# Kernel tuning notes

Hardware: AMD Instinct MI355X
Metric: run time of the kernel (lower is better)

## Reference

```python
import jax, jax.numpy as jnp
import numpy as np

B, D0, D1 = 4096, 128, 128
T, DEPTH, W = 64, 2, 4          # num_tree, depth, width
S = W ** (DEPTH + 1)            # num_state = 64
NODES = sum(W ** l for l in range(DEPTH + 1))  # 21 internal nodes per tree
D = D0 + D1


def setup_inputs() -> dict:
    key = jax.random.key(0)
    ks = jax.random.split(key, 9)
    inp0 = jax.random.normal(ks[0], (B, D0), jnp.float32)
    inp1 = jax.random.normal(ks[1], (B, D1), jnp.float32)
    x2 = jax.random.normal(ks[2], (B,), jnp.float32)
    # ForestLinear: per-tree, per-node linear maps to `width` branch logits
    W_nodes = 0.02 * jax.random.normal(ks[3], (T, NODES, D, W), jnp.float32)
    b_nodes = jnp.zeros((T, NODES, W), jnp.float32)
    # MultiDense([0,1], 1): per-(tree,state) linear probe per input
    W0 = 0.02 * jax.random.normal(ks[4], (T, S, D0), jnp.float32)
    b0 = jnp.zeros((T, S), jnp.float32)
    W1 = 0.02 * jax.random.normal(ks[5], (T, S, D1), jnp.float32)
    b1 = jnp.zeros((T, S), jnp.float32)
    return {"inp0": inp0, "inp1": inp1, "x2": x2,
            "W_nodes": W_nodes, "b_nodes": b_nodes,
            "W0": W0, "b0": b0, "W1": W1, "b1": b1}


def _forest_states(x, W_nodes, b_nodes):
    # x: [B, D] -> leaf-state probabilities [B, T, S]
    logits = jnp.einsum('bd,tndw->btnw', x, W_nodes) + b_nodes  # [B,T,NODES,W]
    probs = jax.nn.softmax(logits, axis=-1)
    p = jnp.ones((x.shape[0], T, 1), probs.dtype)
    off = 0
    for l in range(DEPTH + 1):
        n = W ** l
        pl = probs[:, :, off:off + n, :]                 # [B,T,n,W]
        p = (p[..., None] * pl).reshape(x.shape[0], T, n * W)
        off += n
    return p  # [B, T, S]


def reference(inp0, inp1, x2, W_nodes, b_nodes, W0, b0, W1, b1):
    x_states = _forest_states(jnp.concatenate([inp0, inp1], axis=-1), W_nodes, b_nodes)
    # per-tree/state linear probes; equivalent to tile + MultiDense, no materialized tile
    x_pred = (jnp.einsum('bd,tsd->bts', inp0, W0) + b0
              + jnp.einsum('bd,tsd->bts', inp1, W1) + b1)  # [B,T,S]
    y_pred_logit_parallel = x2[:, None, None] + x_pred
    ave_pred_tree = jnp.sum(x_states * jax.nn.sigmoid(y_pred_logit_parallel), axis=2)  # [B,T]
    ave_pred = jnp.mean(ave_pred_tree, axis=1)  # [B]
    return (y_pred_logit_parallel, ave_pred)
```

## Files before the change

### kernel.cpp

```cpp
#include <hip/hip_runtime.h>

#define B_SZ    4096
#define DD      256
#define T_TREES 64
#define NNODES  21
#define S_LEAF  64
#define M_TILE  128
#define HBYTES  40960
#define WBYTES  (2 * HBYTES)
#define XOFF    ((size_t)T_TREES * WBYTES)
#define QBYTES  20480


typedef __attribute__((ext_vector_type(8))) short  short8;
typedef __attribute__((ext_vector_type(4))) float  f32x4;

#define DPP_ADD(x, ctrl) ((x) + __int_as_float(__builtin_amdgcn_mov_dpp(__float_as_int(x), (ctrl), 0xF, 0xF, true)))
#define DPP_MOV(x, ctrl) __int_as_float(__builtin_amdgcn_mov_dpp(__float_as_int(x), (ctrl), 0xF, 0xF, true))
__device__ __forceinline__ float qsum4(float x) {
    x = DPP_ADD(x, 0xB1);
    x = DPP_ADD(x, 0x4E);
    return x;
}
__device__ __forceinline__ float rsum16(float x) {
    x = DPP_ADD(x, 0xB1);
    x = DPP_ADD(x, 0x4E);
    x = DPP_ADD(x, 0x124);
    x = DPP_ADD(x, 0x128);
    return x;
}

__device__ __forceinline__ unsigned short f2bf(float f) {
    unsigned int u = __float_as_uint(f);
    u += 0x7fffu + ((u >> 16) & 1u);
    return (unsigned short)(u >> 16);
}
__device__ __forceinline__ void gl2lds16(const void* g, void* l) {
    __builtin_amdgcn_global_load_lds(
        (const __attribute__((address_space(1))) unsigned int*)g,
        (__attribute__((address_space(3))) unsigned int*)l, 16, 0, 0);
}
__device__ __host__ __forceinline__ int woffh(int c, int klo) {
    return c * 256 + (((klo ^ c) & 15) << 4);
}
__device__ __host__ __forceinline__ int woffq(int c, int klo) {
    return (c >> 1) * 256 + (((((klo << 1) ^ (c & 14))) | (c & 1)) << 4);
}

__global__ void zero_ave_kernel(float* __restrict__ out1) {
    int i = blockIdx.x * 256 + threadIdx.x;
    if (i < B_SZ) out1[i] = 0.0f;
}

__global__ void prep_weights(const float* __restrict__ Wn, const float* __restrict__ W0,
                             const float* __restrict__ W1, const float* __restrict__ inp0,
                             const float* __restrict__ inp1, char* __restrict__ ws,
                             float* __restrict__ out1) {
    int id = blockIdx.x * 256 + threadIdx.x;
    if (id < 43008) {
        int oct  = id & 31;
        int rest = id >> 5;
        int n    = rest % NNODES;
        int t    = rest / NNODES;
        int h    = oct >> 4, klo = oct & 15;
        const f32x4* src = (const f32x4*)(Wn + (((size_t)t * NNODES + n) * DD + oct * 8) * 4);
        f32x4 v[8];
        #pragma unroll
        for (int j = 0; j < 8; ++j) v[j] = src[j];
        char* base = ws + (size_t)t * WBYTES + h * HBYTES;
        #pragma unroll
        for (int w = 0; w < 4; ++w) {
            int c = n * 4 + w + (n >= 5 ? 12 : 0);
            short8 pack;
            #pragma unroll
            for (int j = 0; j < 8; ++j) pack[j] = (short)f2bf(v[j][w]);
            *(short8*)(base + woffh(c, klo)) = pack;
        }
    } else if (id < 67584) {
        int idx  = id - 43008;
        int kc   = idx & 31;
        int rest = idx >> 5;
        int c    = 20 + rest % 12;
        int t    = rest / 12;
        short8 z = (short8){0,0,0,0,0,0,0,0};
        *(short8*)(ws + (size_t)t * WBYTES + (kc >> 4) * HBYTES + woffh(c, kc & 15)) = z;
    } else if (id < 198656) {
        int idx = id - 67584;
        int kc  = idx & 31;
        int s   = (idx >> 5) & 63;
        int t   = idx >> 11;
        int k0  = kc * 8;
        const float* src = (k0 < 128) ? (W0 + ((size_t)t * S_LEAF + s) * 128 + k0)
                                      : (W1 + ((size_t)t * S_LEAF + s) * 128 + (k0 - 128));
        short8 pack;
        #pragma unroll
        for (int j = 0; j < 8; ++j) pack[j] = (short)f2bf(src[j]);
        *(short8*)(ws + (size_t)t * WBYTES + (kc >> 4) * HBYTES + woffh(96 + s, kc & 15)) = pack;
    } else if (id < 202752) {
        out1[id - 198656] = 0.0f;
    } else if (id < 333824) {
        int idx = id - 202752;
        int oct = idx & 31;
        int r   = idx >> 5;
        const float* src = (oct < 16) ? (inp0 + (size_t)r * 128 + oct * 8)
                                      : (inp1 + (size_t)r * 128 + (oct - 16) * 8);
        f32x4 f0 = *(const f32x4*)src;
        f32x4 f1 = *(const f32x4*)(src + 4);
        short8 pack;
        pack[0]=(short)f2bf(f0[0]); pack[1]=(short)f2bf(f0[1]);
        pack[2]=(short)f2bf(f0[2]); pack[3]=(short)f2bf(f0[3]);
        pack[4]=(short)f2bf(f1[0]); pack[5]=(short)f2bf(f1[1]);
        pack[6]=(short)f2bf(f1[2]); pack[7]=(short)f2bf(f1[3]);
        *(short8*)(ws + XOFF + ((size_t)r * DD + oct * 8) * 2) = pack;
    }
}

__global__ __launch_bounds__(512, 2)
void forest_main(const float* __restrict__ x2,  const float* __restrict__ bn,
                 const float* __restrict__ b0,  const float* __restrict__ b1,
                 const char* __restrict__ wsW,
                 float* __restrict__ out0, float* __restrict__ out1) {
    __shared__ __align__(16) char smem[WBYTES];

    const int tid  = threadIdx.x;
    const int orig = blockIdx.x;
    const int swz  = (orig & 7) * 256 + (orig >> 3);
    const int t    = swz >> 5;
    const int mt   = swz & 31;
    const int m0   = mt * M_TILE;
    const int lane = tid & 63;
    const int wid  = tid >> 6;
    const int ri   = lane & 15;
    const int kg   = lane >> 4;

    const unsigned short* xbf = (const unsigned short*)(wsW + XOFF);
    const char* wbase = wsW + (size_t)t * WBYTES;

    f32x4 acc[10];
    #pragma unroll
    for (int ct = 0; ct < 10; ++ct)
        acc[ct] = (f32x4){0.f, 0.f, 0.f, 0.f};

    const int grr = m0 + wid * 16 + ri;
    const unsigned short* aBase = xbf + (size_t)grr * DD + kg * 8;

    {
        const char* src = wbase + tid * 16;
        char* dst = smem + tid * 16;
        #pragma unroll
        for (int it = 0; it < 10; ++it)
            gl2lds16(src + it * 8192, dst + it * 8192);
    }
    short8 a = *(const short8*)(aBase);
    __syncthreads();

    #pragma unroll
    for (int kk = 0; kk < 8; ++kk) {
        short8 an;
        if (kk < 7)
            an = *(const short8*)(aBase + (kk + 1) * 32);
        const int klo = (kk & 3) * 4 + kg;
        const int dsB = (kk >> 2) * HBYTES + ri * 256 + (((klo ^ ri) & 15) << 4);
        #pragma unroll
        for (int ct = 0; ct < 10; ++ct) {
            short8 bv = *(const short8*)(smem + dsB + ct * 4096);
            acc[ct] = __builtin_amdgcn_mfma_f32_16x16x32_bf16(a, bv, acc[ct], 0, 0, 0);
        }
        a = an;
    }

    const int kgbase = kg * 16;
    {
        const int rlBase = wid * 16 + kg * 4;
        const int gr0 = m0 + rlBase;
        f32x4 x2v = *(const f32x4*)(x2 + gr0);
        float bn0 = bn[t * 84 + ri];
        float bn1 = bn[t * 84 + 16 + (ri & 3)];

        float L1r[4];
        #pragma unroll
        for (int r = 0; r < 4; ++r) {
            float e0 = __expf(acc[0][r] + bn0);
            float p0 = e0 * __builtin_amdgcn_rcpf(qsum4(e0));
            float e1 = __expf(acc[1][r] + bn1);
            float p1 = e1 * __builtin_amdgcn_rcpf(qsum4(e1));
            float pa  = __shfl(p0, kgbase + (ri >> 2));
            float pb0 = DPP_MOV(p0, 0x124);
            float pb1 = DPP_MOV(p1, 0x124);
            L1r[r] = pa * ((ri < 12) ? pb0 : pb1);
        }
        float partial[4] = {0.f, 0.f, 0.f, 0.f};
        #pragma unroll
        for (int ct = 0; ct < 4; ++ct) {
            int s = ct * 16 + ri;
            float bn2 = bn[t * 84 + 20 + s];
            float bb  = b0[t * S_LEAF + s] + b1[t * S_LEAF + s];
            #pragma unroll
            for (int r = 0; r < 4; ++r) {
                float e = __expf(acc[2 + ct][r] + bn2);
                float p2 = e * __builtin_amdgcn_rcpf(qsum4(e));
                float L2 = p2 * __shfl(L1r[r], kgbase + ct * 4 + (ri >> 2));
                float y = acc[6 + ct][r] + x2v[r] + bb;
                out0[((size_t)(gr0 + r) * T_TREES + t) * S_LEAF + s] = y;
                float sg = __builtin_amdgcn_rcpf(1.0f + __expf(-y));
                partial[r] += sg * L2;
            }
        }
        #pragma unroll
        for (int r = 0; r < 4; ++r) {
            float p = rsum16(partial[r]);
            if (ri == 0) atomicAdd(out1 + gr0 + r, p * (1.0f / T_TREES));
        }
    }
}

__device__ __forceinline__ short8 ldAraw(const float* __restrict__ inp0,
                                         const float* __restrict__ inp1,
                                         int gr, int kkidx, int kg) {
    int k0 = kkidx * 32 + kg * 8;
    const float* src = (k0 < 128) ? (inp0 + (size_t)gr * 128 + k0)
                                  : (inp1 + (size_t)gr * 128 + (k0 - 128));
    f32x4 f0 = *(const f32x4*)src;
    f32x4 f1 = *(const f32x4*)(src + 4);
    short8 a;
    a[0]=(short)f2bf(f0[0]); a[1]=(short)f2bf(f0[1]);
    a[2]=(short)f2bf(f0[2]); a[3]=(short)f2bf(f0[3]);
    a[4]=(short)f2bf(f1[0]); a[5]=(short)f2bf(f1[1]);
    a[6]=(short)f2bf(f1[2]); a[7]=(short)f2bf(f1[3]);
    return a;
}

__global__ __launch_bounds__(256, 2)
void forest_fb(const float* __restrict__ inp0, const float* __restrict__ inp1,
               const float* __restrict__ x2,   const float* __restrict__ Wn,
               const float* __restrict__ bn,   const float* __restrict__ W0,
               const float* __restrict__ b0,   const float* __restrict__ W1,
               const float* __restrict__ b1,
               float* __restrict__ out0, float* __restrict__ out1) {
    __shared__ __align__(16) char smem[QBYTES];

    const int tid  = threadIdx.x;
    const int orig = blockIdx.x;
    const int swz  = (orig & 7) * 256 + (orig >> 3);
    const int t    = swz >> 5;
    const int mt   = swz & 31;
    const int m0   = mt * 128;
    const int lane = tid & 63;
    const int wid  = tid >> 6;
    const int ri   = lane & 15;
    const int kg   = lane >> 4;

    f32x4 acc[2][10];
    #pragma unroll
    for (int sr = 0; sr < 2; ++sr)
        #pragma unroll
        for (int ct = 0; ct < 10; ++ct)
            acc[sr][ct] = (f32x4){0.f, 0.f, 0.f, 0.f};

    const int gr0r = m0 + wid * 32 + ri;
    const int gr1r = gr0r + 16;

    int dsb[2];
    #pragma unroll
    for (int kkl = 0; kkl < 2; ++kkl) {
        int klo = kkl * 4 + kg;
        dsb[kkl] = (ri >> 1) * 256 + (((((klo << 1) ^ (ri & 14))) | (ri & 1)) << 4);
    }

    for (int q = 0; q < 4; ++q) {
        #pragma unroll
        for (int it = 0; it < 5; ++it) {
            int idx = tid + it * 256;
            int c   = idx >> 3;
            int klo = idx & 7;
            int k0  = (q * 8 + klo) * 8;
            unsigned short v[8];
            if (c < 20) {
                int n = c >> 2, w = c & 3;
                const float* src = Wn + (((size_t)t * NNODES + n) * DD + k0) * 4 + w;
                #pragma unroll
                for (int j = 0; j < 8; ++j) v[j] = f2bf(src[j * 4]);
            } else if (c < 32) {
                #pragma unroll
                for (int j = 0; j < 8; ++j) v[j] = 0;
            } else if (c < 96) {
                int n = 5 + ((c - 32) >> 2), w = (c - 32) & 3;
                const float* src = Wn + (((size_t)t * NNODES + n) * DD + k0) * 4 + w;
                #pragma unroll
                for (int j = 0; j < 8; ++j) v[j] = f2bf(src[j * 4]);
            } else {
                int s = c - 96;
                const float* src = (k0 < 128) ? (W0 + ((size_t)t * S_LEAF + s) * 128 + k0)
                                              : (W1 + ((size_t)t * S_LEAF + s) * 128 + (k0 - 128));
                #pragma unroll
                for (int j = 0; j < 8; ++j) v[j] = f2bf(src[j]);
            }
            short8 pack;
            #pragma unroll
            for (int j = 0; j < 8; ++j) pack[j] = (short)v[j];
            *(short8*)(smem + woffq(c, klo)) = pack;
        }
        short8 a00 = ldAraw(inp0, inp1, gr0r, 2*q+0, kg);
        short8 a10 = ldAraw(inp0, inp1, gr1r, 2*q+0, kg);
        short8 a01 = ldAraw(inp0, inp1, gr0r, 2*q+1, kg);
        short8 a11 = ldAraw(inp0, inp1, gr1r, 2*q+1, kg);
        __syncthreads();
        #pragma unroll
        for (int ct = 0; ct < 10; ++ct) {
            short8 b0f = *(const short8*)(smem + dsb[0] + ct * 2048);
            acc[0][ct] = __builtin_amdgcn_mfma_f32_16x16x32_bf16(a00, b0f, acc[0][ct], 0, 0, 0);
            acc[1][ct] = __builtin_amdgcn_mfma_f32_16x16x32_bf16(a10, b0f, acc[1][ct], 0, 0, 0);
        }
        #pragma unroll
        for (int ct = 0; ct < 10; ++ct) {
            short8 b1f = *(const short8*)(smem + dsb[1] + ct * 2048);
            acc[0][ct] = __builtin_amdgcn_mfma_f32_16x16x32_bf16(a01, b1f, acc[0][ct], 0, 0, 0);
            acc[1][ct] = __builtin_amdgcn_mfma_f32_16x16x32_bf16(a11, b1f, acc[1][ct], 0, 0, 0);
        }
        if (q < 3) __syncthreads();
    }

    const int kgbase = kg * 16;
    #pragma unroll
    for (int sr = 0; sr < 2; ++sr) {
        const int rlBase = wid * 32 + sr * 16 + kg * 4;
        const int gr0 = m0 + rlBase;
        f32x4 x2v = *(const f32x4*)(x2 + gr0);
        float bn0 = bn[t * 84 + ri];
        float bn1 = bn[t * 84 + 16 + (ri & 3)];
        float L1r[4];
        #pragma unroll
        for (int r = 0; r < 4; ++r) {
            float e0 = __expf(acc[sr][0][r] + bn0);
            float p0 = e0 * __builtin_amdgcn_rcpf(qsum4(e0));
            float e1 = __expf(acc[sr][1][r] + bn1);
            float p1 = e1 * __builtin_amdgcn_rcpf(qsum4(e1));
            float pa  = __shfl(p0, kgbase + (ri >> 2));
            float pb0 = DPP_MOV(p0, 0x124);
            float pb1 = DPP_MOV(p1, 0x124);
            L1r[r] = pa * ((ri < 12) ? pb0 : pb1);
        }
        float partial[4] = {0.f, 0.f, 0.f, 0.f};
        #pragma unroll
        for (int ct = 0; ct < 4; ++ct) {
            int s = ct * 16 + ri;
            float bn2 = bn[t * 84 + 20 + s];
            float bb  = b0[t * S_LEAF + s] + b1[t * S_LEAF + s];
            #pragma unroll
            for (int r = 0; r < 4; ++r) {
                float e = __expf(acc[sr][2 + ct][r] + bn2);
                float p2 = e * __builtin_amdgcn_rcpf(qsum4(e));
                float L2 = p2 * __shfl(L1r[r], kgbase + ct * 4 + (ri >> 2));
                float y = acc[sr][6 + ct][r] + x2v[r] + bb;
                out0[((size_t)(gr0 + r) * T_TREES + t) * S_LEAF + s] = y;
                float sg = __builtin_amdgcn_rcpf(1.0f + __expf(-y));
                partial[r] += sg * L2;
            }
        }
        #pragma unroll
        for (int r = 0; r < 4; ++r) {
            float p = rsum16(partial[r]);
            if (ri == 0) atomicAdd(out1 + gr0 + r, p * (1.0f / T_TREES));
        }
    }
}

extern "C" void kernel_launch(void* const* d_in, const int* in_sizes, int n_in,
                              void* d_out, int out_size, void* d_ws, size_t ws_size,
                              hipStream_t stream) {
    const float* inp0 = (const float*)d_in[0];
    const float* inp1 = (const float*)d_in[1];
    const float* x2   = (const float*)d_in[2];
    const float* Wn   = (const float*)d_in[3];
    const float* bn   = (const float*)d_in[4];
    const float* W0   = (const float*)d_in[5];
    const float* b0   = (const float*)d_in[6];
    const float* W1   = (const float*)d_in[7];
    const float* b1   = (const float*)d_in[8];

    float* out0 = (float*)d_out;
    float* out1 = out0 + (size_t)B_SZ * T_TREES * S_LEAF;

    const size_t need = XOFF + (size_t)B_SZ * DD * 2;
    dim3 grid((B_SZ / M_TILE) * T_TREES);

    if (ws_size >= need) {
        hipLaunchKernelGGL(prep_weights, dim3(1304), dim3(256), 0, stream,
                           Wn, W0, W1, inp0, inp1, (char*)d_ws, out1);
        hipLaunchKernelGGL(forest_main, grid, dim3(512), 0, stream,
                           x2, bn, b0, b1, (const char*)d_ws, out0, out1);
    } else {
        hipLaunchKernelGGL(zero_ave_kernel, dim3((B_SZ + 255) / 256), dim3(256), 0, stream, out1);
        hipLaunchKernelGGL(forest_fb, grid, dim3(256), 0, stream,
                           inp0, inp1, x2, Wn, bn, W0, b0, W1, b1, out0, out1);
    }
}
```

Before: 49.78 us.

## Double-buffer weight staging in K-quarters to halve LDS and raise occupancy

Splits each tree's bf16 weight tile into four K-quarters with a new swizzled layout. The main kernel streams these through two LDS buffers, loading the next quarter while MFMAs run on the current one, instead of loading the whole 80KB tile up front. This halves LDS use per block, which allows the launch bound to request 4 blocks per CU. In exchange it adds extra barriers, each of which also waits on outstanding global loads. The higher occupancy target may also squeeze registers.

After: 49.10 us. No clear change (-1.4%).

```diff
diff --git a/kernel.cpp b/kernel.cpp
--- a/kernel.cpp
+++ b/kernel.cpp
@@ -6,8 +6,8 @@
 #define NNODES  21
 #define S_LEAF  64
 #define M_TILE  128
-#define HBYTES  40960
-#define WBYTES  (2 * HBYTES)
+#define QB      20480
+#define WBYTES  (4 * QB)
 #define XOFF    ((size_t)T_TREES * WBYTES)
 #define QBYTES  20480
 
@@ -40,8 +40,8 @@
         (const __attribute__((address_space(1))) unsigned int*)g,
         (__attribute__((address_space(3))) unsigned int*)l, 16, 0, 0);
 }
-__device__ __host__ __forceinline__ int woffh(int c, int klo) {
-    return c * 256 + (((klo ^ c) & 15) << 4);
+__device__ __host__ __forceinline__ int woffq4(int c, int klo4) {
+    return c * 128 + (((klo4 ^ c) & 7) << 4);
 }
 __device__ __host__ __forceinline__ int woffq(int c, int klo) {
     return (c >> 1) * 256 + (((((klo << 1) ^ (c & 14))) | (c & 1)) << 4);
@@ -62,19 +62,19 @@
         int rest = id >> 5;
         int n    = rest % NNODES;
         int t    = rest / NNODES;
-        int h    = oct >> 4, klo = oct & 15;
+        int q    = oct >> 3, klo4 = oct & 7;
         const f32x4* src = (const f32x4*)(Wn + (((size_t)t * NNODES + n) * DD + oct * 8) * 4);
         f32x4 v[8];
         #pragma unroll
         for (int j = 0; j < 8; ++j) v[j] = src[j];
-        char* base = ws + (size_t)t * WBYTES + h * HBYTES;
+        char* base = ws + (size_t)t * WBYTES + q * QB;
         #pragma unroll
         for (int w = 0; w < 4; ++w) {
             int c = n * 4 + w + (n >= 5 ? 12 : 0);
             short8 pack;
             #pragma unroll
             for (int j = 0; j < 8; ++j) pack[j] = (short)f2bf(v[j][w]);
-            *(short8*)(base + woffh(c, klo)) = pack;
+            *(short8*)(base + woffq4(c, klo4)) = pack;
         }
     } else if (id < 67584) {
         int idx  = id - 43008;
@@ -83,7 +83,7 @@
         int c    = 20 + rest % 12;
         int t    = rest / 12;
         short8 z = (short8){0,0,0,0,0,0,0,0};
-        *(short8*)(ws + (size_t)t * WBYTES + (kc >> 4) * HBYTES + woffh(c, kc & 15)) = z;
+        *(short8*)(ws + (size_t)t * WBYTES + (kc >> 3) * QB + woffq4(c, kc & 7)) = z;
     } else if (id < 198656) {
         int idx = id - 67584;
         int kc  = idx & 31;
@@ -95,7 +95,7 @@
         short8 pack;
         #pragma unroll
         for (int j = 0; j < 8; ++j) pack[j] = (short)f2bf(src[j]);
-        *(short8*)(ws + (size_t)t * WBYTES + (kc >> 4) * HBYTES + woffh(96 + s, kc & 15)) = pack;
+        *(short8*)(ws + (size_t)t * WBYTES + (kc >> 3) * QB + woffq4(96 + s, kc & 7)) = pack;
     } else if (id < 202752) {
         out1[id - 198656] = 0.0f;
     } else if (id < 333824) {
@@ -115,12 +115,12 @@
     }
 }
 
-__global__ __launch_bounds__(512, 2)
+__global__ __launch_bounds__(512, 4)
 void forest_main(const float* __restrict__ x2,  const float* __restrict__ bn,
                  const float* __restrict__ b0,  const float* __restrict__ b1,
                  const char* __restrict__ wsW,
                  float* __restrict__ out0, float* __restrict__ out1) {
-    __shared__ __align__(16) char smem[WBYTES];
+    __shared__ __align__(16) char smem[2 * QB];
 
     const int tid  = threadIdx.x;
     const int orig = blockIdx.x;
@@ -144,26 +144,34 @@
     const int grr = m0 + wid * 16 + ri;
     const unsigned short* aBase = xbf + (size_t)grr * DD + kg * 8;
 
-    {
-        const char* src = wbase + tid * 16;
-        char* dst = smem + tid * 16;
-        #pragma unroll
-        for (int it = 0; it < 10; ++it)
-            gl2lds16(src + it * 8192, dst + it * 8192);
-    }
+    auto stageQ = [&](int q, int buf) {
+        const char* src = wbase + q * QB;
+        char* dst = smem + buf * QB;
+        gl2lds16(src + tid * 16,        dst + tid * 16);
+        gl2lds16(src + 8192 + tid * 16, dst + 8192 + tid * 16);
+        if (tid < 256)
+            gl2lds16(src + 16384 + tid * 16, dst + 16384 + tid * 16);
+    };
+
+    stageQ(0, 0);
     short8 a = *(const short8*)(aBase);
-    __syncthreads();
 
     #pragma unroll
     for (int kk = 0; kk < 8; ++kk) {
+        if ((kk & 1) == 0) {
+            __syncthreads();
+            int q = kk >> 1;
+            if (q < 3) stageQ(q + 1, (q + 1) & 1);
+        }
         short8 an;
         if (kk < 7)
             an = *(const short8*)(aBase + (kk + 1) * 32);
-        const int klo = (kk & 3) * 4 + kg;
-        const int dsB = (kk >> 2) * HBYTES + ri * 256 + (((klo ^ ri) & 15) << 4);
+        const int klo4 = (kk & 1) * 4 + kg;
+        const char* bufp = smem + ((kk >> 1) & 1) * QB;
+        const int dsB = ri * 128 + (((klo4 ^ ri) & 7) << 4);
         #pragma unroll
         for (int ct = 0; ct < 10; ++ct) {
-            short8 bv = *(const short8*)(smem + dsB + ct * 4096);
+            short8 bv = *(const short8*)(bufp + dsB + ct * 2048);
             acc[ct] = __builtin_amdgcn_mfma_f32_16x16x32_bf16(a, bv, acc[ct], 0, 0, 0);
         }
         a = an;
```
